# Kernel tuning notes

Hardware: AMD Instinct MI355X
Metric: run time of the kernel (lower is better)

The kernel has to match this reference:

```python
import jax, jax.numpy as jnp
import numpy as np
from jax import lax


def _conv(x, w, stride=1):
    # x: [N,C,H,W], w: [O,I,k,k]
    return lax.conv_general_dilated(x, w, (stride, stride), 'SAME',
                                    dimension_numbers=('NCHW', 'OIHW', 'NCHW'))


def _up2(x):
    return jnp.repeat(jnp.repeat(x, 2, axis=-2), 2, axis=-1)


def _model(x, Wbs, bbs, Wc1, bc1, Wc2, bc2, Wes, bes):
    h = x
    for W, b in zip(Wbs, bbs):
        h = jax.nn.relu(_conv(h, W, 2) + b[None, :, None, None])
    feats = h  # [B, 512, 4, 4]
    pooled = feats.mean(axis=(2, 3))  # AdaptiveAvgPool2d((1,1)) + Flatten
    hidden = jax.nn.relu(pooled @ Wc1.T + bc1)
    logits = hidden @ Wc2.T + bc2  # [B, 5]
    cls = jnp.argmax(logits, axis=1)  # per-sample expert routing (force_class=None path)

    def expert(f, ws, bs):  # f: [512,4,4]; one sample through its routed UNet decoder
        e = f[None]
        for i in range(5):
            e = _up2(e)
            e = jax.nn.relu(_conv(e, ws[i]) + bs[i][None, :, None, None])
        e = _conv(e, ws[5]) + bs[5][None, :, None, None]  # 1x1 head -> 5 seg channels
        return e[0]

    # MoE-style dispatch: gather each sample's expert weights, then vmap (no per-sample Python loop)
    ws_sel = tuple(W[cls] for W in Wes)  # each [B, co, ci, k, k]
    bs_sel = tuple(b[cls] for b in bes)  # each [B, co]
    seg = jax.vmap(expert)(feats, ws_sel, bs_sel)  # [B, 5, 128, 128]
    return logits, cls, seg


def setup_inputs() -> dict:
    key = jax.random.key(0)
    ks = iter(jax.random.split(key, 48))

    def rn(shape):
        return jax.random.normal(next(ks), shape, dtype=jnp.float32) * 0.05

    B, E = 64, 5
    inp = {"x": jax.random.normal(next(ks), (B, 3, 128, 128), dtype=jnp.float32)}
    for i, (ci, co) in enumerate([(3, 64), (64, 128), (128, 256), (256, 512), (512, 512)], 1):
        inp[f"Wb{i}"] = rn((co, ci, 3, 3))
        inp[f"bb{i}"] = rn((co,))
    inp["Wc1"] = rn((128, 512)); inp["bc1"] = rn((128,))
    inp["Wc2"] = rn((5, 128)); inp["bc2"] = rn((5,))
    for i, (ci, co, k) in enumerate([(512, 256, 3), (256, 128, 3), (128, 64, 3),
                                     (64, 32, 3), (32, 16, 3), (16, 5, 1)], 1):
        inp[f"We{i}"] = rn((E, co, ci, k, k))
        inp[f"be{i}"] = rn((E, co))
    return inp


def reference(x, Wb1, bb1, Wb2, bb2, Wb3, bb3, Wb4, bb4, Wb5, bb5,
              Wc1, bc1, Wc2, bc2,
              We1, be1, We2, be2, We3, be3, We4, be4, We5, be5, We6, be6):
    return _model(x,
                  (Wb1, Wb2, Wb3, Wb4, Wb5), (bb1, bb2, bb3, bb4, bb5),
                  Wc1, bc1, Wc2, bc2,
                  (We1, We2, We3, We4, We5, We6), (be1, be2, be3, be4, be5, be6))
```

## Files before the change

kernel.cpp:

```cpp
#include <hip/hip_runtime.h>
#include <hip/hip_bf16.h>


typedef __attribute__((ext_vector_type(8))) short bf16x8;
typedef __attribute__((ext_vector_type(4))) float f32x4;

static __device__ __forceinline__ unsigned short f2bf(float f) {
    __hip_bfloat16 h = __float2bfloat16(f);
    return *reinterpret_cast<unsigned short*>(&h);
}
static __device__ __forceinline__ float bf2f(unsigned short u) {
    return __uint_as_float(((unsigned int)u) << 16);
}

__global__ __launch_bounds__(256)
void conv1_kernel(const float* __restrict__ in, const float* __restrict__ W,
                  const float* __restrict__ Bias,
                  unsigned short* __restrict__ out_hi,
                  unsigned short* __restrict__ out_lo)
{
    constexpr int R = 17, C = 17;
    __shared__ float ilds[3*R*C];
    __shared__ float wlds[27*32];
    const int n = blockIdx.z, co0 = blockIdx.y*32;
    const int ty = blockIdx.x >> 3, tx = blockIdx.x & 7;
    const int oh0 = ty*8, ow0 = tx*8;
    const int t = threadIdx.x, p = t & 63, grp = t >> 6;
    const int py = p >> 3, px = p & 7;
    const int r0 = 2*oh0, c0 = 2*ow0;

    const float* ibase = in + (long)n*3*16384;
    for (int idx = t; idx < 3*R*C; idx += 256) {
        int ck = idx/(R*C), rc = idx%(R*C);
        int r = rc/C, c = rc%C;
        int ih = r0+r, iw = c0+c;
        float v = 0.f;
        if (ih < 128 && iw < 128) v = ibase[ck*16384 + ih*128 + iw];
        ilds[idx] = v;
    }
    for (int idx = t; idx < 32*27; idx += 256) {
        int co = idx & 31, rem = idx >> 5;
        wlds[rem*32 + co] = W[(co0+co)*27 + rem];
    }
    __syncthreads();

    float acc[8];
    #pragma unroll
    for (int i=0;i<8;i++) acc[i]=0.f;

    #pragma unroll
    for (int ck = 0; ck < 3; ++ck) {
        float xv[9];
        #pragma unroll
        for (int kh = 0; kh < 3; ++kh)
            #pragma unroll
            for (int kw = 0; kw < 3; ++kw)
                xv[kh*3+kw] = ilds[ck*289 + (2*py+kh)*17 + 2*px+kw];
        #pragma unroll
        for (int k = 0; k < 9; ++k) {
            #pragma unroll
            for (int g = 0; g < 2; ++g) {
                const float4 w = *reinterpret_cast<const float4*>(
                    &wlds[(ck*9+k)*32 + grp*8 + g*4]);
                acc[g*4+0] += xv[k]*w.x;
                acc[g*4+1] += xv[k]*w.y;
                acc[g*4+2] += xv[k]*w.z;
                acc[g*4+3] += xv[k]*w.w;
            }
        }
    }

    const long obase = (((long)n*64 + oh0+py)*64 + ow0+px)*64 + co0 + grp*8;
    #pragma unroll
    for (int g = 0; g < 2; ++g) {
        ushort4 sh, sl;
        #pragma unroll
        for (int j = 0; j < 4; ++j) {
            int co = co0 + grp*8 + g*4 + j;
            float v = fmaxf(acc[g*4+j] + Bias[co], 0.f);
            unsigned short h = f2bf(v);
            ((unsigned short*)&sh)[j] = h;
            ((unsigned short*)&sl)[j] = f2bf(v - bf2f(h));
        }
        *reinterpret_cast<ushort4*>(&out_hi[obase + g*4]) = sh;
        *reinterpret_cast<ushort4*>(&out_lo[obase + g*4]) = sl;
    }
}

template<int CI,int CO,int HO,int NW>
__global__ __launch_bounds__(NW*64, 2)
void bb_conv_v3(const unsigned short* __restrict__ in_hi,
                const unsigned short* __restrict__ in_lo,
                const unsigned short* __restrict__ Whi,
                const unsigned short* __restrict__ Wlo,
                const float* __restrict__ Bias,
                unsigned short* __restrict__ out_hi,
                unsigned short* __restrict__ out_lo)
{
    constexpr int HI = HO*2;
    constexpr int R = 17, C = 17;
    constexpr int CK = 32, PITCH = 40;
    constexpr int NTHR = NW*64;

    __shared__ __align__(16) unsigned short xlds[R*C*PITCH];

    const int n   = blockIdx.z;
    const int co0 = blockIdx.y * (NW*64);
    constexpr int TILES_X = HO/8;
    const int ty = blockIdx.x / TILES_X, tx = blockIdx.x % TILES_X;
    const int oh0 = ty*8, ow0 = tx*8;
    const int r0 = 2*oh0, c0 = 2*ow0;

    const int t = threadIdx.x;
    const int w = t >> 6, lane = t & 63;
    const int s = lane & 15, q = lane >> 4;

    int dyy[4], dxx[4];
    #pragma unroll
    for (int si = 0; si < 4; ++si) { dyy[si] = si*2 + (s>>3); dxx[si] = s & 7; }

    const unsigned short* inHn = in_hi + (long)n*HI*HI*CI;
    const unsigned short* inLn = in_lo + (long)n*HI*HI*CI;

    int wrow[4];
    #pragma unroll
    for (int tn = 0; tn < 4; ++tn)
        wrow[tn] = (co0 + w*64 + tn*16 + s)*9*CI + q*8;

    f32x4 acc[4][4];
    #pragma unroll
    for (int si = 0; si < 4; ++si)
        #pragma unroll
        for (int tn = 0; tn < 4; ++tn)
            acc[si][tn] = (f32x4){0.f,0.f,0.f,0.f};

    auto stage = [&](const unsigned short* base, int ci0) {
        for (int i8 = t; i8 < R*C*4; i8 += NTHR) {
            int pix = i8 >> 2, cs = i8 & 3;
            int r = pix / C, c = pix % C;
            int ih = r0 + r, iw = c0 + c;
            uint4 v = {0u,0u,0u,0u};
            if (ih < HI && iw < HI)
                v = *reinterpret_cast<const uint4*>(&base[((long)ih*HI + iw)*CI + ci0 + cs*8]);
            *reinterpret_cast<uint4*>(&xlds[pix*PITCH + cs*8]) = v;
        }
    };

    for (int ci0 = 0; ci0 < CI; ci0 += CK) {
        stage(inHn, ci0);
        __syncthreads();
        {
            bf16x8 ah[2][4], al[2][4];
            #pragma unroll
            for (int tn = 0; tn < 4; ++tn) {
                ah[0][tn] = *reinterpret_cast<const bf16x8*>(&Whi[wrow[tn] + ci0]);
                al[0][tn] = *reinterpret_cast<const bf16x8*>(&Wlo[wrow[tn] + ci0]);
            }
            #pragma unroll
            for (int k = 0; k < 9; ++k) {
                const int cur = k & 1, nxt = cur ^ 1;
                if (k < 8) {
                    #pragma unroll
                    for (int tn = 0; tn < 4; ++tn) {
                        ah[nxt][tn] = *reinterpret_cast<const bf16x8*>(&Whi[wrow[tn] + (k+1)*CI + ci0]);
                        al[nxt][tn] = *reinterpret_cast<const bf16x8*>(&Wlo[wrow[tn] + (k+1)*CI + ci0]);
                    }
                }
                const int kh = k/3, kw = k%3;
                #pragma unroll
                for (int si = 0; si < 4; ++si) {
                    bf16x8 b = *reinterpret_cast<const bf16x8*>(
                        &xlds[((2*dyy[si]+kh)*C + 2*dxx[si]+kw)*PITCH + q*8]);
                    #pragma unroll
                    for (int tn = 0; tn < 4; ++tn) {
                        acc[si][tn] = __builtin_amdgcn_mfma_f32_16x16x32_bf16(ah[cur][tn], b, acc[si][tn], 0,0,0);
                        acc[si][tn] = __builtin_amdgcn_mfma_f32_16x16x32_bf16(al[cur][tn], b, acc[si][tn], 0,0,0);
                    }
                }
            }
        }
        __syncthreads();
        stage(inLn, ci0);
        __syncthreads();
        {
            bf16x8 a2[2][4];
            #pragma unroll
            for (int tn = 0; tn < 4; ++tn)
                a2[0][tn] = *reinterpret_cast<const bf16x8*>(&Whi[wrow[tn] + ci0]);
            #pragma unroll
            for (int k = 0; k < 9; ++k) {
                const int cur = k & 1, nxt = cur ^ 1;
                if (k < 8) {
                    #pragma unroll
                    for (int tn = 0; tn < 4; ++tn)
                        a2[nxt][tn] = *reinterpret_cast<const bf16x8*>(&Whi[wrow[tn] + (k+1)*CI + ci0]);
                }
                const int kh = k/3, kw = k%3;
                #pragma unroll
                for (int si = 0; si < 4; ++si) {
                    bf16x8 b = *reinterpret_cast<const bf16x8*>(
                        &xlds[((2*dyy[si]+kh)*C + 2*dxx[si]+kw)*PITCH + q*8]);
                    #pragma unroll
                    for (int tn = 0; tn < 4; ++tn)
                        acc[si][tn] = __builtin_amdgcn_mfma_f32_16x16x32_bf16(a2[cur][tn], b, acc[si][tn], 0,0,0);
                }
            }
        }
        __syncthreads();
    }

    #pragma unroll
    for (int si = 0; si < 4; ++si) {
        const int oh = oh0 + dyy[si], ow = ow0 + dxx[si];
        #pragma unroll
        for (int tn = 0; tn < 4; ++tn) {
            int co_b = co0 + w*64 + tn*16 + q*4;
            ushort4 sh, sl;
            #pragma unroll
            for (int r = 0; r < 4; ++r) {
                float v = fmaxf(acc[si][tn][r] + Bias[co_b + r], 0.f);
                unsigned short h = f2bf(v);
                ((unsigned short*)&sh)[r] = h;
                ((unsigned short*)&sl)[r] = f2bf(v - bf2f(h));
            }
            long ob = (((long)n*HO + oh)*HO + ow)*CO + co_b;
            *reinterpret_cast<ushort4*>(&out_hi[ob]) = sh;
            *reinterpret_cast<ushort4*>(&out_lo[ob]) = sl;
        }
    }
}

__global__ __launch_bounds__(128, 2)
void conv5_partial(const unsigned short* __restrict__ in_hi,
                   const unsigned short* __restrict__ in_lo,
                   const unsigned short* __restrict__ Whi,
                   const unsigned short* __restrict__ Wlo,
                   float* __restrict__ skbuf)
{
    constexpr int CI = 512, HI = 8;
    constexpr int R = 9, C = 9, CK = 32, PITCH = 40;

    __shared__ __align__(16) unsigned short xlds[4*R*C*PITCH];

    const int sk  = blockIdx.x;
    const int co0 = blockIdx.y * 128;
    const int n0  = blockIdx.z * 4;
    const int t = threadIdx.x;
    const int w = t >> 6, lane = t & 63;
    const int s = lane & 15, q = lane >> 4;
    const int dyy = s >> 2, dxx = s & 3;

    int wrow[4];
    #pragma unroll
    for (int tn = 0; tn < 4; ++tn)
        wrow[tn] = (co0 + w*64 + tn*16 + s)*9*CI + q*8;

    f32x4 acc[4][4];
    #pragma unroll
    for (int si = 0; si < 4; ++si)
        #pragma unroll
        for (int tn = 0; tn < 4; ++tn)
            acc[si][tn] = (f32x4){0.f,0.f,0.f,0.f};

    auto stage = [&](const unsigned short* base, int ci0) {
        for (int i8 = t; i8 < 4*324; i8 += 128) {
            int ti = i8 / 324, rem = i8 % 324;
            int pix = rem >> 2, cs = rem & 3;
            int r = pix / C, c = pix % C;
            uint4 v = {0u,0u,0u,0u};
            if (r < HI && c < HI)
                v = *reinterpret_cast<const uint4*>(
                    &base[(((long)(n0+ti)*HI + r)*HI + c)*CI + ci0 + cs*8]);
            *reinterpret_cast<uint4*>(&xlds[(ti*R*C + pix)*PITCH + cs*8]) = v;
        }
    };

    for (int cc = 0; cc < 64; cc += CK) {
        const int ci0 = sk*64 + cc;
        stage(in_hi, ci0);
        __syncthreads();
        {
            bf16x8 ah[2][4], al[2][4];
            #pragma unroll
            for (int tn = 0; tn < 4; ++tn) {
                ah[0][tn] = *reinterpret_cast<const bf16x8*>(&Whi[wrow[tn] + ci0]);
                al[0][tn] = *reinterpret_cast<const bf16x8*>(&Wlo[wrow[tn] + ci0]);
            }
            #pragma unroll
            for (int k = 0; k < 9; ++k) {
                const int cur = k & 1, nxt = cur ^ 1;
                if (k < 8) {
                    #pragma unroll
                    for (int tn = 0; tn < 4; ++tn) {
                        ah[nxt][tn] = *reinterpret_cast<const bf16x8*>(&Whi[wrow[tn] + (k+1)*CI + ci0]);
                        al[nxt][tn] = *reinterpret_cast<const bf16x8*>(&Wlo[wrow[tn] + (k+1)*CI + ci0]);
                    }
                }
                const int kh = k/3, kw = k%3;
                #pragma unroll
                for (int si = 0; si < 4; ++si) {
                    bf16x8 b = *reinterpret_cast<const bf16x8*>(
                        &xlds[(si*R*C + (2*dyy+kh)*C + 2*dxx+kw)*PITCH + q*8]);
                    #pragma unroll
                    for (int tn = 0; tn < 4; ++tn) {
                        acc[si][tn] = __builtin_amdgcn_mfma_f32_16x16x32_bf16(ah[cur][tn], b, acc[si][tn], 0,0,0);
                        acc[si][tn] = __builtin_amdgcn_mfma_f32_16x16x32_bf16(al[cur][tn], b, acc[si][tn], 0,0,0);
                    }
                }
            }
        }
        __syncthreads();
        stage(in_lo, ci0);
        __syncthreads();
        {
            bf16x8 a2[2][4];
            #pragma unroll
            for (int tn = 0; tn < 4; ++tn)
                a2[0][tn] = *reinterpret_cast<const bf16x8*>(&Whi[wrow[tn] + ci0]);
            #pragma unroll
            for (int k = 0; k < 9; ++k) {
                const int cur = k & 1, nxt = cur ^ 1;
                if (k < 8) {
                    #pragma unroll
                    for (int tn = 0; tn < 4; ++tn)
                        a2[nxt][tn] = *reinterpret_cast<const bf16x8*>(&Whi[wrow[tn] + (k+1)*CI + ci0]);
                }
                const int kh = k/3, kw = k%3;
                #pragma unroll
                for (int si = 0; si < 4; ++si) {
                    bf16x8 b = *reinterpret_cast<const bf16x8*>(
                        &xlds[(si*R*C + (2*dyy+kh)*C + 2*dxx+kw)*PITCH + q*8]);
                    #pragma unroll
                    for (int tn = 0; tn < 4; ++tn)
                        acc[si][tn] = __builtin_amdgcn_mfma_f32_16x16x32_bf16(a2[cur][tn], b, acc[si][tn], 0,0,0);
                }
            }
        }
        __syncthreads();
    }

    #pragma unroll
    for (int si = 0; si < 4; ++si) {
        #pragma unroll
        for (int tn = 0; tn < 4; ++tn) {
            int co_b = co0 + w*64 + tn*16 + q*4;
            long o = (((long)sk*64 + n0+si)*16 + s)*512 + co_b;
            *reinterpret_cast<f32x4*>(&skbuf[o]) = acc[si][tn];
        }
    }
}

__global__ __launch_bounds__(256)
void conv5_reduce(const float* __restrict__ skbuf, const float* __restrict__ Bias,
                  unsigned short* __restrict__ fhi, unsigned short* __restrict__ flo)
{
    int i = blockIdx.x*256 + threadIdx.x;
    int co = i & 511;
    float sacc = Bias[co];
    #pragma unroll
    for (int sk = 0; sk < 8; ++sk) sacc += skbuf[sk*524288 + i];
    float v = fmaxf(sacc, 0.f);
    unsigned short h = f2bf(v);
    fhi[i] = h;
    flo[i] = f2bf(v - bf2f(h));
}

__global__ __launch_bounds__(128, 2)
void dec1_partial(const unsigned short* __restrict__ in,
                  const unsigned short* __restrict__ WT,
                  const int* __restrict__ cls_i,
                  float* __restrict__ dbuf)
{
    constexpr int CI = 512, CO = 256, HI = 4;
    constexpr int R = 6, C = 6, CK = 64, CKQ = 2, PITCH = 72;
    constexpr int NST = 9*CKQ;

    __shared__ __align__(16) unsigned short ilds[R*C*PITCH];

    const int sk  = blockIdx.x;
    const int co0 = blockIdx.y * 128;
    const int n   = blockIdx.z;
    const int e   = cls_i[n];
    const int t = threadIdx.x;
    const int w = t >> 6, lane = t & 63;
    const int s = lane & 15, q = lane >> 4;

    const unsigned short* Wbase = WT + (long)e*CO*9*CI;
    const unsigned short* inN   = in + (long)n*HI*HI*CI;

    int dyy[4], dxx[4];
    #pragma unroll
    for (int si = 0; si < 4; ++si) { dyy[si] = si*2 + (s>>3); dxx[si] = s & 7; }

    long wrow[4];
    #pragma unroll
    for (int tn = 0; tn < 4; ++tn)
        wrow[tn] = (long)(co0 + w*64 + tn*16 + s)*9*CI + q*8;

    f32x4 acc[4][4];
    #pragma unroll
    for (int si = 0; si < 4; ++si)
        #pragma unroll
        for (int tn = 0; tn < 4; ++tn)
            acc[si][tn] = (f32x4){0.f,0.f,0.f,0.f};

    for (int cc = 0; cc < CI/4; cc += CK) {
        const int ci0 = sk*(CI/4) + cc;
        for (int i8 = t; i8 < R*C*8; i8 += 128) {
            int pix = i8 >> 3, cs = i8 & 7;
            int r = pix / C, c = pix % C;
            int ih = r - 1, iw = c - 1;
            uint4 v = {0u,0u,0u,0u};
            if (ih >= 0 && ih < HI && iw >= 0 && iw < HI)
                v = *reinterpret_cast<const uint4*>(&inN[((long)ih*HI + iw)*CI + ci0 + cs*8]);
            *reinterpret_cast<uint4*>(&ilds[pix*PITCH + cs*8]) = v;
        }
        __syncthreads();

        bf16x8 a[3][4];
        #pragma unroll
        for (int pf = 0; pf < 3; ++pf) {
            const int kp = pf/CKQ, cp = pf%CKQ;
            #pragma unroll
            for (int tn = 0; tn < 4; ++tn)
                a[pf][tn] = *reinterpret_cast<const bf16x8*>(&Wbase[wrow[tn] + kp*CI + ci0 + cp*32]);
        }
        #pragma unroll
        for (int st = 0; st < NST; ++st) {
            const int slot = st % 3;
            bf16x8 acur[4];
            #pragma unroll
            for (int tn = 0; tn < 4; ++tn) acur[tn] = a[slot][tn];
            if (st + 3 < NST) {
                const int kp = (st+3)/CKQ, cp = (st+3)%CKQ;
                #pragma unroll
                for (int tn = 0; tn < 4; ++tn)
                    a[slot][tn] = *reinterpret_cast<const bf16x8*>(&Wbase[wrow[tn] + kp*CI + ci0 + cp*32]);
            }
            const int k = st/CKQ, ckq = st%CKQ;
            const int kh = k/3, kw = k%3;
            #pragma unroll
            for (int si = 0; si < 4; ++si) {
                const int ihr = ((dyy[si] + kh - 1) >> 1) + 1;
                const int iwr = ((dxx[si] + kw - 1) >> 1) + 1;
                bf16x8 b = *reinterpret_cast<const bf16x8*>(
                    &ilds[(ihr*C + iwr)*PITCH + ckq*32 + q*8]);
                #pragma unroll
                for (int tn = 0; tn < 4; ++tn)
                    acc[si][tn] = __builtin_amdgcn_mfma_f32_16x16x32_bf16(acur[tn], b, acc[si][tn], 0, 0, 0);
            }
        }
        __syncthreads();
    }

    #pragma unroll
    for (int si = 0; si < 4; ++si) {
        int px = dyy[si]*8 + dxx[si];
        #pragma unroll
        for (int tn = 0; tn < 4; ++tn) {
            int co_b = co0 + w*64 + tn*16 + q*4;
            long o = (((long)sk*64 + n)*64 + px)*256 + co_b;
            *reinterpret_cast<f32x4*>(&dbuf[o]) = acc[si][tn];
        }
    }
}

__global__ __launch_bounds__(256)
void dec1_reduce(const float* __restrict__ dbuf, const float* __restrict__ be1,
                 const int* __restrict__ cls_i, unsigned short* __restrict__ P)
{
    int i = blockIdx.x*256 + threadIdx.x;
    int n = i >> 14;
    int co = i & 255;
    int e = cls_i[n];
    float sacc = be1[e*256 + co];
    #pragma unroll
    for (int sk = 0; sk < 4; ++sk) sacc += dbuf[sk*1048576 + i];
    P[i] = f2bf(fmaxf(sacc, 0.f));
}

template<int CI>
__device__ __forceinline__ void trans_split_row(const float* __restrict__ src,
                                                unsigned short* __restrict__ hi,
                                                unsigned short* __restrict__ lo,
                                                int blk, float* buf, int t)
{
    const float* sp = src + (long)blk*(CI*9);
    for (int i = t; i < CI*9; i += 256) buf[i] = sp[i];
    __syncthreads();
// ... 188 lines not shown
                const int iwr = ((dxx[si] + kw - 1) >> 1) + 1;
                bf16x8 b = *reinterpret_cast<const bf16x8*>(
                    &ilds[(ihr*C + iwr)*PITCH + ckq*32 + q*8]);
                #pragma unroll
                for (int tn = 0; tn < 4; ++tn)
                    acc[si][tn] = __builtin_amdgcn_mfma_f32_16x16x32_bf16(acur[tn], b, acc[si][tn], 0, 0, 0);
            }
        }
        __syncthreads();
    }

    #pragma unroll
    for (int si = 0; si < 4; ++si) {
        int oh = oh0 + dyy[si], ow = ow0 + dxx[si];
        #pragma unroll
        for (int tn = 0; tn < 4; ++tn) {
            int co_b = co0 + w*64 + tn*16 + q*4;
            ushort4 st4;
            #pragma unroll
            for (int r = 0; r < 4; ++r) {
                float v = acc[si][tn][r] + Be[e*CO + co_b + r];
                v = fmaxf(v, 0.f);
                ((unsigned short*)&st4)[r] = f2bf(v);
            }
            *reinterpret_cast<ushort4*>(&out[(((long)n*HO + oh)*HO + ow)*CO + co_b]) = st4;
        }
    }
}

template<int CI,int CO,int HO,int TH,int TW,int CO_T,int CK>
__global__ __launch_bounds__(256, 2)
void dec_conv_kernel(const unsigned short* __restrict__ in,
                     const unsigned short* __restrict__ WT,
                     const float* __restrict__ Be,
                     const int* __restrict__ cls_i,
                     unsigned short* __restrict__ out)
{
    constexpr int HI = HO/2;
    constexpr int R = TH/2 + 2, C = TW/2 + 2;
    constexpr int PITCH = CK + 8;
    constexpr int NT = CO_T/16;
    constexpr int S  = (TH*TW)/64;
    constexpr int SXT = TW/8;
    constexpr int CKQ = CK/32;
    constexpr int NST = 9*CKQ;

    __shared__ __align__(16) unsigned short ilds[R*C*PITCH];

    const int n = blockIdx.z;
    const int e = cls_i[n];
    const int co0 = blockIdx.y * CO_T;
    constexpr int TILES_X = HO/TW;
    const int ty = blockIdx.x / TILES_X, tx = blockIdx.x % TILES_X;
    const int oh0 = ty*TH, ow0 = tx*TW;
    const int ih0 = oh0/2 - 1, iw0 = ow0/2 - 1;

    const int t = threadIdx.x;
    const int w = t >> 6;
    const int lane = t & 63;
    const int s = lane & 15;
    const int q = lane >> 4;

    const unsigned short* Wbase = WT + ((long)e*CO + co0)*9*CI;
    const unsigned short* inN   = in + (long)n*HI*HI*CI;

    long wrow[NT];
    #pragma unroll
    for (int tn = 0; tn < NT; ++tn)
        wrow[tn] = (long)(tn*16 + s)*9*CI + q*8;

    f32x4 acc[S][NT];
    #pragma unroll
    for (int si = 0; si < S; ++si)
        #pragma unroll
        for (int tn = 0; tn < NT; ++tn)
            acc[si][tn] = (f32x4){0.f,0.f,0.f,0.f};

    int dy[S], dx[S];
    #pragma unroll
    for (int si = 0; si < S; ++si) {
        int sub = w + si*4;
        int sy = sub / SXT, sx = sub % SXT;
        dy[si] = sy*2 + (s >> 3);
        dx[si] = sx*8 + (s & 7);
    }

    for (int ci0 = 0; ci0 < CI; ci0 += CK) {
        constexpr int C8 = CK/8;
        for (int i8 = t; i8 < R*C*C8; i8 += 256) {
            int pix = i8 / C8, cs = i8 % C8;
            int r = pix / C, c = pix % C;
            int ih = ih0 + r, iw = iw0 + c;
            uint4 v = {0u,0u,0u,0u};
            if (ih >= 0 && ih < HI && iw >= 0 && iw < HI)
                v = *reinterpret_cast<const uint4*>(&inN[((long)ih*HI + iw)*CI + ci0 + cs*8]);
            *reinterpret_cast<uint4*>(&ilds[pix*PITCH + cs*8]) = v;
        }
        __syncthreads();

        bf16x8 a[3][NT];
        #pragma unroll
        for (int pf = 0; pf < 3 && pf < NST; ++pf) {
            const int kp = pf/CKQ, cp = pf%CKQ;
            #pragma unroll
            for (int tn = 0; tn < NT; ++tn)
                a[pf][tn] = *reinterpret_cast<const bf16x8*>(&Wbase[wrow[tn] + kp*CI + ci0 + cp*32]);
        }
        #pragma unroll
        for (int st = 0; st < NST; ++st) {
            const int slot = st % 3;
            bf16x8 acur[NT];
            #pragma unroll
            for (int tn = 0; tn < NT; ++tn) acur[tn] = a[slot][tn];
            if (st + 3 < NST) {
                const int kp = (st+3)/CKQ, cp = (st+3)%CKQ;
                #pragma unroll
                for (int tn = 0; tn < NT; ++tn)
                    a[slot][tn] = *reinterpret_cast<const bf16x8*>(&Wbase[wrow[tn] + kp*CI + ci0 + cp*32]);
            }
            const int k = st/CKQ, ckq = st%CKQ;
            const int kh = k/3, kw = k%3;
            #pragma unroll
            for (int si = 0; si < S; ++si) {
                int ihr = ((dy[si] + kh - 1) >> 1) + 1;
                int iwr = ((dx[si] + kw - 1) >> 1) + 1;
                bf16x8 b = *reinterpret_cast<const bf16x8*>(
                    &ilds[(ihr*C + iwr)*PITCH + ckq*32 + q*8]);
                #pragma unroll
                for (int tn = 0; tn < NT; ++tn)
                    acc[si][tn] = __builtin_amdgcn_mfma_f32_16x16x32_bf16(acur[tn], b, acc[si][tn], 0, 0, 0);
            }
        }
        __syncthreads();
    }

    #pragma unroll
    for (int si = 0; si < S; ++si) {
        int oh = oh0 + dy[si], ow = ow0 + dx[si];
        #pragma unroll
        for (int tn = 0; tn < NT; ++tn) {
            int co_b = co0 + tn*16 + q*4;
            ushort4 st4;
            #pragma unroll
            for (int r = 0; r < 4; ++r) {
                float v = acc[si][tn][r] + Be[e*CO + co_b + r];
                v = fmaxf(v, 0.f);
                ((unsigned short*)&st4)[r] = f2bf(v);
            }
            *reinterpret_cast<ushort4*>(&out[(((long)n*HO + oh)*HO + ow)*CO + co_b]) = st4;
        }
    }
}

__global__ __launch_bounds__(256) void head_kernel(const unsigned short* __restrict__ d5,
                                                   const float* __restrict__ Wh,
                                                   const float* __restrict__ bh,
                                                   const int* __restrict__ cls_i,
                                                   float* __restrict__ seg)
{
    int n = blockIdx.y;
    int p = blockIdx.x*256 + threadIdx.x;
    __shared__ float w[85];
    int e = cls_i[n];
    if (threadIdx.x < 80) w[threadIdx.x] = Wh[(long)e*80 + threadIdx.x];
    if (threadIdx.x < 5)  w[80+threadIdx.x] = bh[e*5 + threadIdx.x];
    __syncthreads();
    const unsigned short* dp = d5 + ((long)n*16384 + p)*16;
    uint4 u0 = *reinterpret_cast<const uint4*>(dp);
    uint4 u1 = *reinterpret_cast<const uint4*>(dp + 8);
    float x[16];
    unsigned int uu[4] = {u0.x, u0.y, u0.z, u0.w};
    unsigned int vv[4] = {u1.x, u1.y, u1.z, u1.w};
    #pragma unroll
    for (int i = 0; i < 4; ++i) {
        x[2*i+0] = __uint_as_float(uu[i] << 16);
        x[2*i+1] = __uint_as_float(uu[i] & 0xffff0000u);
        x[8+2*i+0] = __uint_as_float(vv[i] << 16);
        x[8+2*i+1] = __uint_as_float(vv[i] & 0xffff0000u);
    }
    #pragma unroll
    for (int co = 0; co < 5; ++co) {
        float sacc = w[80+co];
        #pragma unroll
        for (int ci = 0; ci < 16; ++ci) sacc += x[ci]*w[co*16+ci];
        seg[((long)n*5 + co)*16384 + p] = sacc;
    }
}

extern "C" void kernel_launch(void* const* d_in, const int* in_sizes, int n_in,
                              void* d_out, int out_size, void* d_ws, size_t ws_size,
                              hipStream_t stream)
{
    const float* x   = (const float*)d_in[0];
    const float* Wb1 = (const float*)d_in[1];  const float* bb1 = (const float*)d_in[2];
    const float* Wb2 = (const float*)d_in[3];  const float* bb2 = (const float*)d_in[4];
    const float* Wb3 = (const float*)d_in[5];  const float* bb3 = (const float*)d_in[6];
    const float* Wb4 = (const float*)d_in[7];  const float* bb4 = (const float*)d_in[8];
    const float* Wb5 = (const float*)d_in[9];  const float* bb5 = (const float*)d_in[10];
    const float* Wc1 = (const float*)d_in[11]; const float* bc1 = (const float*)d_in[12];
    const float* Wc2 = (const float*)d_in[13]; const float* bc2 = (const float*)d_in[14];
    const float* We1 = (const float*)d_in[15]; const float* be1 = (const float*)d_in[16];
    const float* We2 = (const float*)d_in[17]; const float* be2 = (const float*)d_in[18];
    const float* We3 = (const float*)d_in[19]; const float* be3 = (const float*)d_in[20];
    const float* We4 = (const float*)d_in[21]; const float* be4 = (const float*)d_in[22];
    const float* We5 = (const float*)d_in[23]; const float* be5 = (const float*)d_in[24];
    const float* We6 = (const float*)d_in[25]; const float* be6 = (const float*)d_in[26];

    float* out = (float*)d_out;
    char* ws = (char*)d_ws;

    unsigned short* H1hi = (unsigned short*)(ws + 0);
    unsigned short* H1lo = (unsigned short*)(ws + 33554432);
    unsigned short* H3hi = (unsigned short*)(ws + 0);
    unsigned short* H3lo = (unsigned short*)(ws + 8388608);
    unsigned short* WB4hi = (unsigned short*)(ws + 16777216);
    unsigned short* WB4lo = (unsigned short*)(ws + 19136512);
    unsigned short* WB5hi = (unsigned short*)(ws + 21495808);
    unsigned short* WB5lo = (unsigned short*)(ws + 26214400);
    float*          SKBUF5 = (float*)(ws + 0);
    unsigned short* P    = (unsigned short*)(ws + 0);
    unsigned short* Q    = (unsigned short*)(ws + 33554432);
    float*          DBUF1 = (float*)(ws + 33554432);
    unsigned short* WT1  = (unsigned short*)(ws + 50331648);
    unsigned short* WT2  = (unsigned short*)(ws + 62128128);
    unsigned short* WT3  = (unsigned short*)(ws + 65077248);
    unsigned short* WT4  = (unsigned short*)(ws + 65814528);
    unsigned short* WT5  = (unsigned short*)(ws + 65998848);

    char* Y = ws + 67108864;
    unsigned short* H2hi = (unsigned short*)(Y + 0);
    unsigned short* H2lo = (unsigned short*)(Y + 16777216);
    unsigned short* H4hi = (unsigned short*)(Y + 0);
    unsigned short* H4lo = (unsigned short*)(Y + 4194304);
    unsigned short* FShi = (unsigned short*)(Y + 8388608);
    unsigned short* FSlo = (unsigned short*)(Y + 9437184);
    int*   cls_i  = (int*)(Y + 10649600);

    char* W23 = ws + 100663296;
    unsigned short* WB2hi = (unsigned short*)(W23 + 0);
    unsigned short* WB2lo = (unsigned short*)(W23 + 147456);
    unsigned short* WB3hi = (unsigned short*)(W23 + 294912);
    unsigned short* WB3lo = (unsigned short*)(W23 + 884736);

    hipLaunchKernelGGL(early_trans_kernel, dim3(384), dim3(256), 0, stream,
                       Wb2, Wb3, WB2hi, WB2lo, WB3hi, WB3lo);

    hipLaunchKernelGGL(conv1_kernel, dim3(64,2,64), dim3(256), 0, stream, x, Wb1, bb1, H1hi, H1lo);

    hipLaunchKernelGGL((bb_conv_v3<64,128,32,2>), dim3(16,1,64), dim3(128), 0, stream,
                       H1hi, H1lo, WB2hi, WB2lo, bb2, H2hi, H2lo);

    hipLaunchKernelGGL(late_trans_kernel, dim3(3504), dim3(256), 0, stream,
                       Wb4, Wb5, We1, We2, We3, We4, We5,
                       WB4hi, WB4lo, WB5hi, WB5lo, WT1, WT2, WT3, WT4, WT5);

    hipLaunchKernelGGL((bb_conv_v3<128,256,16,2>), dim3(4,2,64), dim3(128), 0, stream,
                       H2hi, H2lo, WB3hi, WB3lo, bb3, H3hi, H3lo);
    hipLaunchKernelGGL((bb_conv_v3<256,512, 8,2>), dim3(1,4,64), dim3(128), 0, stream,
                       H3hi, H3lo, WB4hi, WB4lo, bb4, H4hi, H4lo);

    hipLaunchKernelGGL(conv5_partial, dim3(8,4,16), dim3(128), 0, stream,
                       H4hi, H4lo, WB5hi, WB5lo, SKBUF5);
    hipLaunchKernelGGL(conv5_reduce, dim3(2048), dim3(256), 0, stream,
                       SKBUF5, bb5, FShi, FSlo);

    hipLaunchKernelGGL(classifier_kernel, dim3(64), dim3(128), 0, stream,
                       FShi, FSlo, Wc1, bc1, Wc2, bc2, out, cls_i);

    hipLaunchKernelGGL(dec1_partial, dim3(4,2,64), dim3(128), 0, stream,
                       FShi, WT1, cls_i, DBUF1);
    hipLaunchKernelGGL(dec1_reduce, dim3(4096), dim3(256), 0, stream,
                       DBUF1, be1, cls_i, P);

    hipLaunchKernelGGL((dec_conv_v2<256,128, 16,2>), dim3(4, 1,64), dim3(128), 0, stream, P, WT2, be2, cls_i, Q);
    hipLaunchKernelGGL((dec_conv_v2<128, 64, 32,1>), dim3(16,1,64), dim3(64),  0, stream, Q, WT3, be3, cls_i, P);
    hipLaunchKernelGGL((dec_conv_kernel< 64, 32, 64, 16,16, 32,64>), dim3(16, 1,64), dim3(256), 0, stream, P, WT4, be4, cls_i, Q);
    hipLaunchKernelGGL((dec_conv_kernel< 32, 16,128, 16,32, 16,32>), dim3(32, 1,64), dim3(256), 0, stream, Q, WT5, be5, cls_i, P);

    hipLaunchKernelGGL(head_kernel, dim3(64,64), dim3(256), 0, stream, P, We6, be6, cls_i, out + 384);
}
```

Before: 748.0 us.

## Stage hi/lo activations together in backbone convs and fuse dec5 with head

```diff
diff --git a/kernel.cpp b/kernel.cpp
--- a/kernel.cpp
+++ b/kernel.cpp
@@ -87,9 +87,9 @@
     }
 }
 
-template<int CI,int CO,int HO,int NW>
+template<int CI,int CO,int HO,int NW,int NPACK>
 __global__ __launch_bounds__(NW*64, 2)
-void bb_conv_v3(const unsigned short* __restrict__ in_hi,
+void bb_conv_v2(const unsigned short* __restrict__ in_hi,
                 const unsigned short* __restrict__ in_lo,
                 const unsigned short* __restrict__ Whi,
                 const unsigned short* __restrict__ Wlo,
@@ -98,29 +98,34 @@
                 unsigned short* __restrict__ out_lo)
 {
     constexpr int HI = HO*2;
-    constexpr int R = 17, C = 17;
-    constexpr int CK = 32, PITCH = 40;
-    constexpr int NTHR = NW*64;
-
-    __shared__ __align__(16) unsigned short xlds[R*C*PITCH];
-
-    const int n   = blockIdx.z;
-    const int co0 = blockIdx.y * (NW*64);
-    constexpr int TILES_X = HO/8;
+    constexpr int TH = (NPACK==1) ? 8 : 4;
+    constexpr int TW = TH;
+    constexpr int R  = 2*TH+1, C = 2*TW+1;
+    constexpr int CK = 32;
+    constexpr int PITCH = CK + 8;
+    constexpr int CO_T  = NW*64;
+    constexpr int NTHR  = NW*64;
+
+    __shared__ __align__(16) unsigned short hi_lds[NPACK*R*C*PITCH];
+    __shared__ __align__(16) unsigned short lo_lds[NPACK*R*C*PITCH];
+
+    const int n0  = blockIdx.z * NPACK;
+    const int co0 = blockIdx.y * CO_T;
+    constexpr int TILES_X = (NPACK==1) ? (HO/TW) : 1;
     const int ty = blockIdx.x / TILES_X, tx = blockIdx.x % TILES_X;
-    const int oh0 = ty*8, ow0 = tx*8;
+    const int oh0 = ty*TH, ow0 = tx*TW;
     const int r0 = 2*oh0, c0 = 2*ow0;
 
     const int t = threadIdx.x;
     const int w = t >> 6, lane = t & 63;
     const int s = lane & 15, q = lane >> 4;
 
-    int dyy[4], dxx[4];
-    #pragma unroll
-    for (int si = 0; si < 4; ++si) { dyy[si] = si*2 + (s>>3); dxx[si] = s & 7; }
-
-    const unsigned short* inHn = in_hi + (long)n*HI*HI*CI;
-    const unsigned short* inLn = in_lo + (long)n*HI*HI*CI;
+    int dyy[4], dxx[4], tb[4];
+    #pragma unroll
+    for (int si = 0; si < 4; ++si) {
+        if (NPACK == 1) { dyy[si] = si*2 + (s>>3); dxx[si] = s & 7; tb[si] = 0; }
+        else            { dyy[si] = s >> 2;        dxx[si] = s & 3; tb[si] = si*R*C*PITCH; }
+    }
 
     int wrow[4];
     #pragma unroll
@@ -134,84 +139,68 @@
         for (int tn = 0; tn < 4; ++tn)
             acc[si][tn] = (f32x4){0.f,0.f,0.f,0.f};
 
-    auto stage = [&](const unsigned short* base, int ci0) {
-        for (int i8 = t; i8 < R*C*4; i8 += NTHR) {
-            int pix = i8 >> 2, cs = i8 & 3;
+    for (int ci0 = 0; ci0 < CI; ci0 += CK) {
+        constexpr int C8  = CK/8;
+        constexpr int PXW = R*C*C8;
+        for (int i8 = t; i8 < NPACK*PXW; i8 += NTHR) {
+            int ti = i8 / PXW, rem = i8 % PXW;
+            int pix = rem / C8, cs = rem % C8;
             int r = pix / C, c = pix % C;
             int ih = r0 + r, iw = c0 + c;
-            uint4 v = {0u,0u,0u,0u};
-            if (ih < HI && iw < HI)
-                v = *reinterpret_cast<const uint4*>(&base[((long)ih*HI + iw)*CI + ci0 + cs*8]);
-            *reinterpret_cast<uint4*>(&xlds[pix*PITCH + cs*8]) = v;
-        }
-    };
-
-    for (int ci0 = 0; ci0 < CI; ci0 += CK) {
-        stage(inHn, ci0);
+            uint4 vh = {0u,0u,0u,0u}, vl = {0u,0u,0u,0u};
+            if (ih < HI && iw < HI) {
+                long off = (((long)(n0+ti)*HI + ih)*HI + iw)*CI + ci0 + cs*8;
+                vh = *reinterpret_cast<const uint4*>(&in_hi[off]);
+                vl = *reinterpret_cast<const uint4*>(&in_lo[off]);
+            }
+            *reinterpret_cast<uint4*>(&hi_lds[(ti*R*C + pix)*PITCH + cs*8]) = vh;
+            *reinterpret_cast<uint4*>(&lo_lds[(ti*R*C + pix)*PITCH + cs*8]) = vl;
+        }
         __syncthreads();
-        {
-            bf16x8 ah[2][4], al[2][4];
-            #pragma unroll
-            for (int tn = 0; tn < 4; ++tn) {
-                ah[0][tn] = *reinterpret_cast<const bf16x8*>(&Whi[wrow[tn] + ci0]);
-                al[0][tn] = *reinterpret_cast<const bf16x8*>(&Wlo[wrow[tn] + ci0]);
-            }
-            #pragma unroll
-            for (int k = 0; k < 9; ++k) {
-                const int cur = k & 1, nxt = cur ^ 1;
-                if (k < 8) {
-                    #pragma unroll
-                    for (int tn = 0; tn < 4; ++tn) {
-                        ah[nxt][tn] = *reinterpret_cast<const bf16x8*>(&Whi[wrow[tn] + (k+1)*CI + ci0]);
-                        al[nxt][tn] = *reinterpret_cast<const bf16x8*>(&Wlo[wrow[tn] + (k+1)*CI + ci0]);
-                    }
+
+        bf16x8 ah[2][4], al[2][4];
+        #pragma unroll
+        for (int tn = 0; tn < 4; ++tn) {
+            const int wo = wrow[tn] + ci0;
+            ah[0][tn] = *reinterpret_cast<const bf16x8*>(&Whi[wo]);
+            al[0][tn] = *reinterpret_cast<const bf16x8*>(&Wlo[wo]);
+        }
+        #pragma unroll
+        for (int k = 0; k < 9; ++k) {
+            const int cur = k & 1, nxt = cur ^ 1;
+            if (k < 8) {
+                #pragma unroll
+                for (int tn = 0; tn < 4; ++tn) {
+                    const int wo = wrow[tn] + (k+1)*CI + ci0;
+                    ah[nxt][tn] = *reinterpret_cast<const bf16x8*>(&Whi[wo]);
+                    al[nxt][tn] = *reinterpret_cast<const bf16x8*>(&Wlo[wo]);
                 }
-                const int kh = k/3, kw = k%3;
+            }
+            const int kh = k/3, kw = k%3;
+            bf16x8 bh[4], bl[4];
+            #pragma unroll
+            for (int si = 0; si < 4; ++si) {
+                const int pi = tb[si] + ((2*dyy[si]+kh)*C + 2*dxx[si]+kw)*PITCH + q*8;
+                bh[si] = *reinterpret_cast<const bf16x8*>(&hi_lds[pi]);
+                bl[si] = *reinterpret_cast<const bf16x8*>(&lo_lds[pi]);
+            }
+            #pragma unroll
+            for (int si = 0; si < 4; ++si)
                 #pragma unroll
-                for (int si = 0; si < 4; ++si) {
-                    bf16x8 b = *reinterpret_cast<const bf16x8*>(
-                        &xlds[((2*dyy[si]+kh)*C + 2*dxx[si]+kw)*PITCH + q*8]);
-                    #pragma unroll
-                    for (int tn = 0; tn < 4; ++tn) {
-                        acc[si][tn] = __builtin_amdgcn_mfma_f32_16x16x32_bf16(ah[cur][tn], b, acc[si][tn], 0,0,0);
-                        acc[si][tn] = __builtin_amdgcn_mfma_f32_16x16x32_bf16(al[cur][tn], b, acc[si][tn], 0,0,0);
-                    }
+                for (int tn = 0; tn < 4; ++tn) {
+                    acc[si][tn] = __builtin_amdgcn_mfma_f32_16x16x32_bf16(ah[cur][tn], bh[si], acc[si][tn], 0,0,0);
+                    acc[si][tn] = __builtin_amdgcn_mfma_f32_16x16x32_bf16(ah[cur][tn], bl[si], acc[si][tn], 0,0,0);
+                    acc[si][tn] = __builtin_amdgcn_mfma_f32_16x16x32_bf16(al[cur][tn], bh[si], acc[si][tn], 0,0,0);
                 }
-            }
         }
         __syncthreads();
-        stage(inLn, ci0);
-        __syncthreads();
-        {
-            bf16x8 a2[2][4];
-            #pragma unroll
-            for (int tn = 0; tn < 4; ++tn)
-                a2[0][tn] = *reinterpret_cast<const bf16x8*>(&Whi[wrow[tn] + ci0]);
-            #pragma unroll
-            for (int k = 0; k < 9; ++k) {
-                const int cur = k & 1, nxt = cur ^ 1;
-                if (k < 8) {
-                    #pragma unroll
-                    for (int tn = 0; tn < 4; ++tn)
-                        a2[nxt][tn] = *reinterpret_cast<const bf16x8*>(&Whi[wrow[tn] + (k+1)*CI + ci0]);
-                }
-                const int kh = k/3, kw = k%3;
-                #pragma unroll
-                for (int si = 0; si < 4; ++si) {
-                    bf16x8 b = *reinterpret_cast<const bf16x8*>(
-                        &xlds[((2*dyy[si]+kh)*C + 2*dxx[si]+kw)*PITCH + q*8]);
-                    #pragma unroll
-                    for (int tn = 0; tn < 4; ++tn)
-                        acc[si][tn] = __builtin_amdgcn_mfma_f32_16x16x32_bf16(a2[cur][tn], b, acc[si][tn], 0,0,0);
-                }
-            }
-        }
-        __syncthreads();
     }
 
     #pragma unroll
     for (int si = 0; si < 4; ++si) {
-        const int oh = oh0 + dyy[si], ow = ow0 + dxx[si];
+        const int n_s = (NPACK==1) ? n0 : (n0 + si);
+        const int oh  = (NPACK==1) ? (oh0 + dyy[si]) : dyy[si];
+        const int ow  = (NPACK==1) ? (ow0 + dxx[si]) : dxx[si];
         #pragma unroll
         for (int tn = 0; tn < 4; ++tn) {
             int co_b = co0 + w*64 + tn*16 + q*4;
@@ -223,7 +212,7 @@
                 ((unsigned short*)&sh)[r] = h;
                 ((unsigned short*)&sl)[r] = f2bf(v - bf2f(h));
             }
-            long ob = (((long)n*HO + oh)*HO + ow)*CO + co_b;
+            long ob = (((long)n_s*HO + oh)*HO + ow)*CO + co_b;
             *reinterpret_cast<ushort4*>(&out_hi[ob]) = sh;
             *reinterpret_cast<ushort4*>(&out_lo[ob]) = sl;
         }
@@ -240,7 +229,8 @@
     constexpr int CI = 512, HI = 8;
     constexpr int R = 9, C = 9, CK = 32, PITCH = 40;
 
-    __shared__ __align__(16) unsigned short xlds[4*R*C*PITCH];
+    __shared__ __align__(16) unsigned short hi_lds[4*R*C*PITCH];
+    __shared__ __align__(16) unsigned short lo_lds[4*R*C*PITCH];
 
     const int sk  = blockIdx.x;
     const int co0 = blockIdx.y * 128;
@@ -262,79 +252,57 @@
         for (int tn = 0; tn < 4; ++tn)
             acc[si][tn] = (f32x4){0.f,0.f,0.f,0.f};
 
-    auto stage = [&](const unsigned short* base, int ci0) {
+    for (int cc = 0; cc < 64; cc += CK) {
+        const int ci0 = sk*64 + cc;
         for (int i8 = t; i8 < 4*324; i8 += 128) {
             int ti = i8 / 324, rem = i8 % 324;
             int pix = rem >> 2, cs = rem & 3;
             int r = pix / C, c = pix % C;
-            uint4 v = {0u,0u,0u,0u};
-            if (r < HI && c < HI)
-                v = *reinterpret_cast<const uint4*>(
-                    &base[(((long)(n0+ti)*HI + r)*HI + c)*CI + ci0 + cs*8]);
-            *reinterpret_cast<uint4*>(&xlds[(ti*R*C + pix)*PITCH + cs*8]) = v;
-        }
-    };
-
-    for (int cc = 0; cc < 64; cc += CK) {
-        const int ci0 = sk*64 + cc;
-        stage(in_hi, ci0);
+            uint4 vh = {0u,0u,0u,0u}, vl = {0u,0u,0u,0u};
+            if (r < HI && c < HI) {
+                long off = (((long)(n0+ti)*HI + r)*HI + c)*CI + ci0 + cs*8;
+                vh = *reinterpret_cast<const uint4*>(&in_hi[off]);
+                vl = *reinterpret_cast<const uint4*>(&in_lo[off]);
+            }
+            *reinterpret_cast<uint4*>(&hi_lds[(ti*R*C + pix)*PITCH + cs*8]) = vh;
+            *reinterpret_cast<uint4*>(&lo_lds[(ti*R*C + pix)*PITCH + cs*8]) = vl;
+        }
         __syncthreads();
-        {
-            bf16x8 ah[2][4], al[2][4];
-            #pragma unroll
-            for (int tn = 0; tn < 4; ++tn) {
-                ah[0][tn] = *reinterpret_cast<const bf16x8*>(&Whi[wrow[tn] + ci0]);
-                al[0][tn] = *reinterpret_cast<const bf16x8*>(&Wlo[wrow[tn] + ci0]);
-            }
-            #pragma unroll
-            for (int k = 0; k < 9; ++k) {
-                const int cur = k & 1, nxt = cur ^ 1;
-                if (k < 8) {
-                    #pragma unroll
-                    for (int tn = 0; tn < 4; ++tn) {
-                        ah[nxt][tn] = *reinterpret_cast<const bf16x8*>(&Whi[wrow[tn] + (k+1)*CI + ci0]);
-                        al[nxt][tn] = *reinterpret_cast<const bf16x8*>(&Wlo[wrow[tn] + (k+1)*CI + ci0]);
-                    }
+
+        bf16x8 ah[2][4], al[2][4];
+        #pragma unroll
+        for (int tn = 0; tn < 4; ++tn) {
+            const int wo = wrow[tn] + ci0;
+            ah[0][tn] = *reinterpret_cast<const bf16x8*>(&Whi[wo]);
+            al[0][tn] = *reinterpret_cast<const bf16x8*>(&Wlo[wo]);
+        }
+        #pragma unroll
+        for (int k = 0; k < 9; ++k) {
+            const int cur = k & 1, nxt = cur ^ 1;
+            if (k < 8) {
+                #pragma unroll
+                for (int tn = 0; tn < 4; ++tn) {
+                    const int wo = wrow[tn] + (k+1)*CI + ci0;
+                    ah[nxt][tn] = *reinterpret_cast<const bf16x8*>(&Whi[wo]);
+                    al[nxt][tn] = *reinterpret_cast<const bf16x8*>(&Wlo[wo]);
                 }
-                const int kh = k/3, kw = k%3;
+            }
+            const int kh = k/3, kw = k%3;
+            bf16x8 bh[4], bl[4];
+            #pragma unroll
+            for (int si = 0; si < 4; ++si) {
+                const int pi = si*R*C*PITCH + ((2*dyy+kh)*C + 2*dxx+kw)*PITCH + q*8;
+                bh[si] = *reinterpret_cast<const bf16x8*>(&hi_lds[pi]);
+                bl[si] = *reinterpret_cast<const bf16x8*>(&lo_lds[pi]);
+            }
+            #pragma unroll
+            for (int si = 0; si < 4; ++si)
                 #pragma unroll
-                for (int si = 0; si < 4; ++si) {
-                    bf16x8 b = *reinterpret_cast<const bf16x8*>(
-                        &xlds[(si*R*C + (2*dyy+kh)*C + 2*dxx+kw)*PITCH + q*8]);
-                    #pragma unroll
-                    for (int tn = 0; tn < 4; ++tn) {
-                        acc[si][tn] = __builtin_amdgcn_mfma_f32_16x16x32_bf16(ah[cur][tn], b, acc[si][tn], 0,0,0);
-                        acc[si][tn] = __builtin_amdgcn_mfma_f32_16x16x32_bf16(al[cur][tn], b, acc[si][tn], 0,0,0);
-                    }
+                for (int tn = 0; tn < 4; ++tn) {
+                    acc[si][tn] = __builtin_amdgcn_mfma_f32_16x16x32_bf16(ah[cur][tn], bh[si], acc[si][tn], 0,0,0);
+                    acc[si][tn] = __builtin_amdgcn_mfma_f32_16x16x32_bf16(ah[cur][tn], bl[si], acc[si][tn], 0,0,0);
+                    acc[si][tn] = __builtin_amdgcn_mfma_f32_16x16x32_bf16(al[cur][tn], bh[si], acc[si][tn], 0,0,0);
                 }
-            }
-        }
-        __syncthreads();
-        stage(in_lo, ci0);
-        __syncthreads();
-        {
-            bf16x8 a2[2][4];
-            #pragma unroll
-            for (int tn = 0; tn < 4; ++tn)
-                a2[0][tn] = *reinterpret_cast<const bf16x8*>(&Whi[wrow[tn] + ci0]);
-            #pragma unroll
-            for (int k = 0; k < 9; ++k) {
-                const int cur = k & 1, nxt = cur ^ 1;
-                if (k < 8) {
-                    #pragma unroll
-                    for (int tn = 0; tn < 4; ++tn)
-                        a2[nxt][tn] = *reinterpret_cast<const bf16x8*>(&Whi[wrow[tn] + (k+1)*CI + ci0]);
-                }
-                const int kh = k/3, kw = k%3;
-                #pragma unroll
-                for (int si = 0; si < 4; ++si) {
-                    bf16x8 b = *reinterpret_cast<const bf16x8*>(
-                        &xlds[(si*R*C + (2*dyy+kh)*C + 2*dxx+kw)*PITCH + q*8]);
-                    #pragma unroll
-                    for (int tn = 0; tn < 4; ++tn)
-                        acc[si][tn] = __builtin_amdgcn_mfma_f32_16x16x32_bf16(a2[cur][tn], b, acc[si][tn], 0,0,0);
-                }
-            }
         }
         __syncthreads();
     }
@@ -829,38 +797,112 @@
     }
 }
 
-__global__ __launch_bounds__(256) void head_kernel(const unsigned short* __restrict__ d5,
-                                                   const float* __restrict__ Wh,
-                                                   const float* __restrict__ bh,
-                                                   const int* __restrict__ cls_i,
-                                                   float* __restrict__ seg)
-{
-    int n = blockIdx.y;
-    int p = blockIdx.x*256 + threadIdx.x;
-    __shared__ float w[85];
-    int e = cls_i[n];
-    if (threadIdx.x < 80) w[threadIdx.x] = Wh[(long)e*80 + threadIdx.x];
-    if (threadIdx.x < 5)  w[80+threadIdx.x] = bh[e*5 + threadIdx.x];
-    __syncthreads();
-    const unsigned short* dp = d5 + ((long)n*16384 + p)*16;
-    uint4 u0 = *reinterpret_cast<const uint4*>(dp);
-    uint4 u1 = *reinterpret_cast<const uint4*>(dp + 8);
-    float x[16];
-    unsigned int uu[4] = {u0.x, u0.y, u0.z, u0.w};
-    unsigned int vv[4] = {u1.x, u1.y, u1.z, u1.w};
-    #pragma unroll
-    for (int i = 0; i < 4; ++i) {
-        x[2*i+0] = __uint_as_float(uu[i] << 16);
-        x[2*i+1] = __uint_as_float(uu[i] & 0xffff0000u);
-        x[8+2*i+0] = __uint_as_float(vv[i] << 16);
-        x[8+2*i+1] = __uint_as_float(vv[i] & 0xffff0000u);
-    }
-    #pragma unroll
-    for (int co = 0; co < 5; ++co) {
-        float sacc = w[80+co];
-        #pragma unroll
-        for (int ci = 0; ci < 16; ++ci) sacc += x[ci]*w[co*16+ci];
-        seg[((long)n*5 + co)*16384 + p] = sacc;
+__global__ __launch_bounds__(256, 2)
+void dec5_head_kernel(const unsigned short* __restrict__ in,
+                      const unsigned short* __restrict__ WT,
+                      const float* __restrict__ be5,
+                      const float* __restrict__ We6,
+                      const float* __restrict__ be6,
+                      const int* __restrict__ cls_i,
+                      float* __restrict__ seg)
+{
+    constexpr int CI = 32, CO = 16, HO = 128, TH = 16, TW = 32, CK = 32;
+    constexpr int HI = 64, R = TH/2 + 2, C = TW/2 + 2, PITCH = CK + 8;
+    constexpr int S = (TH*TW)/64, SXT = TW/8;
+    constexpr int NST = 9;
+
+    __shared__ __align__(16) unsigned short ilds[R*C*PITCH];
+    __shared__ float hw[85];
+
+    const int n = blockIdx.z;
+    const int e = cls_i[n];
+    constexpr int TILES_X = HO/TW;
+    const int ty = blockIdx.x / TILES_X, tx = blockIdx.x % TILES_X;
+    const int oh0 = ty*TH, ow0 = tx*TW;
+    const int ih0 = oh0/2 - 1, iw0 = ow0/2 - 1;
+
+    const int t = threadIdx.x;
+    const int w = t >> 6, lane = t & 63;
+    const int s = lane & 15, q = lane >> 4;
+
+    if (t < 80) hw[t] = We6[(long)e*80 + t];
+    if (t < 5)  hw[80+t] = be6[e*5 + t];
+
+    const unsigned short* Wbase = WT + (long)e*CO*9*CI;
+    const unsigned short* inN   = in + (long)n*HI*HI*CI;
+
+    long wrow = (long)s*9*CI + q*8;
+
+    f32x4 acc[S];
+    #pragma unroll
+    for (int si = 0; si < S; ++si) acc[si] = (f32x4){0.f,0.f,0.f,0.f};
+
+    int dy[S], dx[S];
+    #pragma unroll
+    for (int si = 0; si < S; ++si) {
+        int sub = w + si*4;
+        int sy = sub / SXT, sx = sub % SXT;
+        dy[si] = sy*2 + (s >> 3);
+        dx[si] = sx*8 + (s & 7);
+    }
+
+    {
+        constexpr int C8 = CK/8;
+        for (int i8 = t; i8 < R*C*C8; i8 += 256) {
+            int pix = i8 / C8, cs = i8 % C8;
+            int r = pix / C, c = pix % C;
+            int ih = ih0 + r, iw = iw0 + c;
+            uint4 v = {0u,0u,0u,0u};
+            if (ih >= 0 && ih < HI && iw >= 0 && iw < HI)
+                v = *reinterpret_cast<const uint4*>(&inN[((long)ih*HI + iw)*CI + cs*8]);
+            *reinterpret_cast<uint4*>(&ilds[pix*PITCH + cs*8]) = v;
+        }
+        __syncthreads();
+
+        bf16x8 a[3];
+        #pragma unroll
+        for (int pf = 0; pf < 3; ++pf)
+            a[pf] = *reinterpret_cast<const bf16x8*>(&Wbase[wrow + pf*CI]);
+        #pragma unroll
+        for (int st = 0; st < NST; ++st) {
+            const int slot = st % 3;
+            bf16x8 acur = a[slot];
+            if (st + 3 < NST)
+                a[slot] = *reinterpret_cast<const bf16x8*>(&Wbase[wrow + (st+3)*CI]);
+            const int kh = st/3, kw = st%3;
+            #pragma unroll
+            for (int si = 0; si < S; ++si) {
+                int ihr = ((dy[si] + kh - 1) >> 1) + 1;
+                int iwr = ((dx[si] + kw - 1) >> 1) + 1;
+                bf16x8 b = *reinterpret_cast<const bf16x8*>(
+                    &ilds[(ihr*C + iwr)*PITCH + q*8]);
+                acc[si] = __builtin_amdgcn_mfma_f32_16x16x32_bf16(acur, b, acc[si], 0, 0, 0);
+            }
+        }
+    }
+
+    #pragma unroll
+    for (int si = 0; si < S; ++si) {
+        float v[4];
+        #pragma unroll
+        for (int r = 0; r < 4; ++r)
+            v[r] = fmaxf(acc[si][r] + be5[e*16 + q*4 + r], 0.f);
+        float part[5];
+        #pragma unroll
+        for (int c = 0; c < 5; ++c)
+            part[c] = v[0]*hw[c*16 + q*4] + v[1]*hw[c*16 + q*4 + 1]
+                    + v[2]*hw[c*16 + q*4 + 2] + v[3]*hw[c*16 + q*4 + 3];
+        #pragma unroll
+        for (int c = 0; c < 5; ++c) {
+            part[c] += __shfl_xor(part[c], 16, 64);
+            part[c] += __shfl_xor(part[c], 32, 64);
+        }
+        if (q == 0) {
+            int oh = oh0 + dy[si], ow = ow0 + dx[si];
+            #pragma unroll
+            for (int c = 0; c < 5; ++c)
+                seg[(((long)n*5 + c)*128 + oh)*128 + ow] = part[c] + hw[80+c];
+        }
     }
 }
 
@@ -924,16 +966,16 @@
 
     hipLaunchKernelGGL(conv1_kernel, dim3(64,2,64), dim3(256), 0, stream, x, Wb1, bb1, H1hi, H1lo);
 
-    hipLaunchKernelGGL((bb_conv_v3<64,128,32,2>), dim3(16,1,64), dim3(128), 0, stream,
+    hipLaunchKernelGGL((bb_conv_v2<64,128,32,2,1>), dim3(16,1,64), dim3(128), 0, stream,
                        H1hi, H1lo, WB2hi, WB2lo, bb2, H2hi, H2lo);
 
     hipLaunchKernelGGL(late_trans_kernel, dim3(3504), dim3(256), 0, stream,
                        Wb4, Wb5, We1, We2, We3, We4, We5,
                        WB4hi, WB4lo, WB5hi, WB5lo, WT1, WT2, WT3, WT4, WT5);
 
-    hipLaunchKernelGGL((bb_conv_v3<128,256,16,2>), dim3(4,2,64), dim3(128), 0, stream,
+    hipLaunchKernelGGL((bb_conv_v2<128,256,16,2,1>), dim3(4,2,64), dim3(128), 0, stream,
                        H2hi, H2lo, WB3hi, WB3lo, bb3, H3hi, H3lo);
-    hipLaunchKernelGGL((bb_conv_v3<256,512, 8,2>), dim3(1,4,64), dim3(128), 0, stream,
+    hipLaunchKernelGGL((bb_conv_v2<256,512, 8,2,1>), dim3(1,4,64), dim3(128), 0, stream,
                        H3hi, H3lo, WB4hi, WB4lo, bb4, H4hi, H4lo);
 
     hipLaunchKernelGGL(conv5_partial, dim3(8,4,16), dim3(128), 0, stream,
@@ -952,7 +994,7 @@
     hipLaunchKernelGGL((dec_conv_v2<256,128, 16,2>), dim3(4, 1,64), dim3(128), 0, stream, P, WT2, be2, cls_i, Q);
     hipLaunchKernelGGL((dec_conv_v2<128, 64, 32,1>), dim3(16,1,64), dim3(64),  0, stream, Q, WT3, be3, cls_i, P);
     hipLaunchKernelGGL((dec_conv_kernel< 64, 32, 64, 16,16, 32,64>), dim3(16, 1,64), dim3(256), 0, stream, P, WT4, be4, cls_i, Q);
-    hipLaunchKernelGGL((dec_conv_kernel< 32, 16,128, 16,32, 16,32>), dim3(32, 1,64), dim3(256), 0, stream, Q, WT5, be5, cls_i, P);
-
-    hipLaunchKernelGGL(head_kernel, dim3(64,64), dim3(256), 0, stream, P, We6, be6, cls_i, out + 384);
-}
+
+    hipLaunchKernelGGL(dec5_head_kernel, dim3(32,1,64), dim3(256), 0, stream,
+                       Q, WT5, be5, We6, be6, cls_i, out + 384);
+}
```

Measured after the change: 649.2 us. -13.2%, faster.
